# Kernel optimization log

Hardware: AMD Instinct MI355X
Metric: run time of the kernel (lower is better)

## Reference

```python
import jax, jax.numpy as jnp
import numpy as np

HEADS = 4
DIM_HEAD = 32
SCALE = DIM_HEAD ** -0.5


def setup_inputs() -> dict:
    key = jax.random.key(0)
    ks = jax.random.split(key, 7)
    b, c, h, w = 2, 256, 64, 64
    time_dim = 512
    hidden = HEADS * DIM_HEAD  # 128
    return {
        "x": jax.random.normal(ks[0], (b, c, h, w), jnp.float32),
        "time_emb": jax.random.normal(ks[1], (b, time_dim), jnp.float32),
        "w_mlp": jax.random.normal(ks[2], (2 * c, time_dim), jnp.float32) * 0.02,
        "b_mlp": jax.random.normal(ks[3], (2 * c,), jnp.float32) * 0.02,
        "w_qkv": jax.random.normal(ks[4], (3 * hidden, c), jnp.float32) * 0.05,
        "w_out": jax.random.normal(ks[5], (c, hidden), jnp.float32) * 0.05,
        "b_out": jax.random.normal(ks[6], (c,), jnp.float32) * 0.02,
    }


def reference(x, time_emb, w_mlp, b_mlp, w_qkv, w_out, b_out):
    b, c, h, w = x.shape
    n = h * w
    # FiLM conditioning: SiLU -> Linear -> chunk into (scale, shift)
    t = jax.nn.silu(time_emb) @ w_mlp.T + b_mlp            # [b, 2c]
    scale, shift = jnp.split(t, 2, axis=1)                  # [b, c] each
    x = x * (scale + 1.0)[:, :, None, None] + shift[:, :, None, None]
    # 1x1 conv QKV projection (no bias)
    qkv = jnp.einsum('oc,bchw->bohw', w_qkv, x)             # [b, 3*hidden, h, w]
    q, k, v = jnp.split(qkv, 3, axis=1)                     # [b, hidden, h, w]
    def to_heads(t):
        return t.reshape(b, HEADS, DIM_HEAD, n)             # b h d (x y)
    q, k, v = to_heads(q) * SCALE, to_heads(k), to_heads(v)
    sim = jnp.einsum('bhdi,bhdj->bhij', q, k)               # [b, h, n, n]
    attn = jax.nn.softmax(sim, axis=-1)
    out = jnp.einsum('bhij,bhdj->bhid', attn, v)            # [b, h, n, d]
    # b h (x y) d -> b (h d) x y
    out = out.transpose(0, 1, 3, 2).reshape(b, HEADS * DIM_HEAD, h, w)
    return jnp.einsum('oc,bchw->bohw', w_out, out) + b_out[None, :, None, None]
```

## Files before the change

kernel.cpp:

```cpp
#include <hip/hip_runtime.h>


typedef __bf16 bf16x8 __attribute__((ext_vector_type(8)));
typedef float  f32x16 __attribute__((ext_vector_type(16)));
typedef unsigned uint2v __attribute__((ext_vector_type(2)));

#define MFMA(a, b, c) __builtin_amdgcn_mfma_f32_32x32x16_bf16((a), (b), (c), 0, 0, 0)
#define PLSWAP(a, b) __builtin_amdgcn_permlane32_swap((a), (b), false, false)

static constexpr float kLOG2E = 1.4426950408889634f;
static constexpr float kSCALE = 0.17677669529663687f;

__device__ __forceinline__ unsigned short bf16r(float x) {
  union { float f; unsigned u; } v; v.f = x;
  return (unsigned short)((v.u + 0x7FFFu + ((v.u >> 16) & 1u)) >> 16);
}
__device__ __forceinline__ float fast_silu(float x) {
  return x / (1.0f + __builtin_amdgcn_exp2f(-x * kLOG2E));
}
__device__ __forceinline__ f32x16 zero16() {
  f32x16 z;
#pragma unroll
  for (int i = 0; i < 16; ++i) z[i] = 0.0f;
  return z;
}
__device__ __forceinline__ bf16x8 ld_frag(const unsigned short* p) {
  return *reinterpret_cast<const bf16x8*>(p);
}
__device__ __forceinline__ bf16x8 ld_lds_frag(const unsigned short* p) {
  union { unsigned long long q[2]; bf16x8 v; } u;
  u.q[0] = *(const unsigned long long*)(p);
  u.q[1] = *(const unsigned long long*)(p + 4);
  return u.v;
}

__global__ __launch_bounds__(256) void prep(const float* __restrict__ x,
                                            unsigned short* __restrict__ xT,
                                            const float* __restrict__ te,
                                            const float* __restrict__ w_mlp,
                                            const float* __restrict__ b_mlp,
                                            float* __restrict__ fparams) {
  __shared__ unsigned short lds[64][66];
  int bid = blockIdx.x;
  if (bid < 32) {
    int g = bid * 256 + threadIdx.x;
    int pair = g >> 3, ks = g & 7;
    int b = pair >> 9, o = pair & 511;
    const float4* w4 = (const float4*)(w_mlp + (size_t)o * 512 + ks * 64);
    const float4* t4 = (const float4*)(te + (size_t)b * 512 + ks * 64);
    float s = 0.0f;
#pragma unroll 4
    for (int k = 0; k < 16; ++k) {
      float4 wv = w4[k];
      float4 tv = t4[k];
      s += wv.x * fast_silu(tv.x) + wv.y * fast_silu(tv.y) +
           wv.z * fast_silu(tv.z) + wv.w * fast_silu(tv.w);
    }
    s += __shfl_xor(s, 1, 64);
    s += __shfl_xor(s, 2, 64);
    s += __shfl_xor(s, 4, 64);
    if (ks == 0) {
      float t_val = s + b_mlp[o];
      fparams[b * 512 + o] = (o < 256) ? (t_val + 1.0f) : t_val;
    }
    return;
  }
  int bid2 = bid - 32;
  int p0 = (bid2 & 63) * 64;
  int c0 = ((bid2 >> 6) & 3) * 64;
  int b  = bid2 >> 8;
  int t = threadIdx.x;
  int pl = t & 63, cw = t >> 6;
  const float* xb = x + ((size_t)b * 256 + c0) * 4096 + p0;
#pragma unroll
  for (int r = 0; r < 16; ++r) {
    int cl = cw + r * 4;
    lds[pl][cl] = bf16r(xb[(size_t)cl * 4096 + pl]);
  }
  __syncthreads();
  unsigned short* out = xT + ((size_t)b * 4096 + p0) * 256 + c0;
#pragma unroll
  for (int rep = 0; rep < 2; ++rep) {
    int ch = t + rep * 256;
    int pr = ch >> 3, cc = (ch & 7) * 8;
    union { unsigned short u[8]; uint4 v; } pk;
#pragma unroll
    for (int i = 0; i < 8; ++i) pk.u[i] = lds[pr][cc + i];
    *(uint4*)(out + (size_t)pr * 256 + cc) = pk.v;
  }
}

__global__ __launch_bounds__(256) void film2(const float* __restrict__ w_qkv,
                                             const float* __restrict__ fparams,
                                             const float* __restrict__ w_out,
                                             unsigned short* __restrict__ Aeff,
                                             float* __restrict__ qb,
                                             unsigned short* __restrict__ WoBf) {
  int tid = blockIdx.x * 256 + threadIdx.x;
  if (tid < 24576) {
    int row = tid >> 5, cs = tid & 31;
    int b = row / 384, o = row % 384;
    float qs = (o < 128) ? (kSCALE * kLOG2E) : 1.0f;
    const float4* wr  = (const float4*)(w_qkv + (size_t)o * 256);
    const float4* sc4 = (const float4*)(fparams + b * 512);
    const float4* sh4 = (const float4*)(fparams + b * 512 + 256);
    unsigned short* arow = Aeff + ((size_t)b * 384 + o) * 256;
    float acc = 0.0f;
#pragma unroll
    for (int j = 0; j < 2; ++j) {
      int c4 = cs * 2 + j;
      float4 wv = wr[c4], scv = sc4[c4], shv = sh4[c4];
      acc += wv.x * shv.x + wv.y * shv.y + wv.z * shv.z + wv.w * shv.w;
      union { unsigned short u[4]; unsigned long long q; } pk;
      pk.u[0] = bf16r(wv.x * scv.x * qs);
      pk.u[1] = bf16r(wv.y * scv.y * qs);
      pk.u[2] = bf16r(wv.z * scv.z * qs);
      pk.u[3] = bf16r(wv.w * scv.w * qs);
      *(unsigned long long*)(arow + c4 * 4) = pk.q;
    }
    acc += __shfl_xor(acc, 1, 64);
    acc += __shfl_xor(acc, 2, 64);
    acc += __shfl_xor(acc, 4, 64);
    acc += __shfl_xor(acc, 8, 64);
    acc += __shfl_xor(acc, 16, 64);
    if (cs == 0) qb[b * 384 + o] = acc * qs;
  } else {
    int t = tid - 24576;
    const float4* src = (const float4*)(w_out + (size_t)t * 64);
    unsigned short* dst = WoBf + (size_t)t * 64;
#pragma unroll 4
    for (int i = 0; i < 16; ++i) {
      float4 v = src[i];
      union { unsigned short u[4]; unsigned long long q; } pk;
      pk.u[0] = bf16r(v.x); pk.u[1] = bf16r(v.y);
      pk.u[2] = bf16r(v.z); pk.u[3] = bf16r(v.w);
      *(unsigned long long*)(dst + i * 4) = pk.q;
    }
  }
}

__global__ __launch_bounds__(64) void qkv_gemm(const unsigned short* __restrict__ Aeff,
                                               const float* __restrict__ qb,
                                               const unsigned short* __restrict__ xT,
                                               unsigned short* __restrict__ Qb,
                                               unsigned short* __restrict__ Kb,
                                               unsigned short* __restrict__ Vt) {
  int bid = blockIdx.x;
  int o_blk = bid % 12;
  int rest = bid / 12;
  int b = rest & 1, p_blk = rest >> 1;
  int l = threadIdx.x, col = l & 31, hi = l >> 5;

  const unsigned short* Ab = Aeff + ((size_t)b * 384 + o_blk * 32) * 256;
  const unsigned short* Bb = xT + ((size_t)b * 4096 + p_blk * 32) * 256;

  f32x16 acc = zero16();
#pragma unroll
  for (int kc = 0; kc < 256; kc += 16) {
    bf16x8 a0 = ld_frag(Ab + (size_t)col * 256 + kc + hi * 8);
    bf16x8 b0 = ld_frag(Bb + (size_t)col * 256 + kc + hi * 8);
    acc = MFMA(a0, b0, acc);
  }

  int obase = o_blk * 32;
  int sec = obase >> 7;
  int head = (obase & 127) >> 5;
  size_t bh = (size_t)b * 4 + head;
  int p = p_blk * 32 + col;
  if (sec < 2) {
    unsigned short* dst = (sec == 0 ? Qb : Kb) + (bh * 4096 + p) * 32;
#pragma unroll
    for (int g = 0; g < 4; ++g) {
      int dbase = 8 * g + 4 * hi;
      union { unsigned short u[4]; unsigned long long q; } pk;
#pragma unroll
      for (int r = 0; r < 4; ++r)
        pk.u[r] = bf16r(acc[4 * g + r] + qb[b * 384 + obase + dbase + r]);
      *(unsigned long long*)(dst + dbase) = pk.q;
    }
  } else {
    unsigned short* dst = Vt + bh * 131072 + (size_t)p_blk * 1024;
#pragma unroll
    for (int reg = 0; reg < 16; ++reg) {
      int d = (reg & 3) + 8 * (reg >> 2) + 4 * hi;
      dst[d * 32 + col] = bf16r(acc[reg] + qb[b * 384 + obase + d]);
    }
  }
}

__device__ __forceinline__ void softmax_pv(f32x16 S, bf16x8 va0, bf16x8 va1,
                                           f32x16& O, float& lsum) {
#pragma unroll
  for (int i = 0; i < 16; ++i) S[i] = __builtin_amdgcn_exp2f(S[i]);
  float s0 = (S[0] + S[1]) + (S[2] + S[3]);
  float s1 = (S[4] + S[5]) + (S[6] + S[7]);
  float s2 = (S[8] + S[9]) + (S[10] + S[11]);
  float s3 = (S[12] + S[13]) + (S[14] + S[15]);
  lsum += (s0 + s1) + (s2 + s3);
  union { __bf16 h[16]; unsigned u[8]; } pu;
#pragma unroll
  for (int i = 0; i < 16; ++i) pu.h[i] = (__bf16)S[i];
  uint2v r0 = PLSWAP(pu.u[0], pu.u[2]);
  uint2v r1 = PLSWAP(pu.u[1], pu.u[3]);
  uint2v r2 = PLSWAP(pu.u[4], pu.u[6]);
  uint2v r3 = PLSWAP(pu.u[5], pu.u[7]);
  union { unsigned u[4]; bf16x8 v; } B0, B1;
  B0.u[0] = r0[0]; B0.u[1] = r1[0]; B0.u[2] = r0[1]; B0.u[3] = r1[1];
  B1.u[0] = r2[0]; B1.u[1] = r3[0]; B1.u[2] = r2[1]; B1.u[3] = r3[1];
  O = MFMA(va0, B0.v, O);
  O = MFMA(va1, B1.v, O);
}

__global__ __launch_bounds__(256, 4) void attn(const unsigned short* __restrict__ Qb,
                                               const unsigned short* __restrict__ Kb,
                                               const unsigned short* __restrict__ Vt,
                                               float* __restrict__ Opart,
                                               float* __restrict__ Lpart) {
  __shared__ unsigned short kv[2][2][32][36];

  int bid = blockIdx.x;
  int qblk = bid & 15;
  int ks   = (bid >> 4) & 7;
  int bh   = bid >> 7;
  int t = threadIdx.x;
  int w = t >> 6, l = t & 63, col = l & 31, hi = l >> 5;

  int q0 = qblk * 256 + w * 64;
  const unsigned short* Qp = Qb + ((size_t)bh * 4096 + q0) * 32;
  bf16x8 qf0 = ld_frag(Qp + col * 32 + hi * 8);
  bf16x8 qf1 = ld_frag(Qp + col * 32 + 16 + hi * 8);
  bf16x8 qg0 = ld_frag(Qp + (col + 32) * 32 + hi * 8);
  bf16x8 qg1 = ld_frag(Qp + (col + 32) * 32 + 16 + hi * 8);

  int sec = t >> 7, rr = (t & 127) >> 2, cc = t & 3;
  const unsigned short* gsrc =
      (sec ? Vt : Kb) + (size_t)bh * 131072 + ks * 16384 + (t & 127) * 8;

  const f32x16 zc = zero16();
  f32x16 Oa = zero16(), Obb = zero16();
  float lsuma = 0.0f, lsumb = 0.0f;

  uint4 greg = *(const uint4*)(gsrc);

  for (int tt = 0; tt < 16; ++tt) {
    __syncthreads();
    int buf = tt & 1;
    unsigned short* d0 = &kv[buf][sec][rr][cc * 8];
    *(unsigned long long*)(d0)     = ((const unsigned long long*)&greg)[0];
    *(unsigned long long*)(d0 + 4) = ((const unsigned long long*)&greg)[1];
    if (tt < 15) greg = *(const uint4*)(gsrc + (tt + 1) * 1024);
    __syncthreads();

    bf16x8 ka0 = ld_lds_frag(&kv[buf][0][col][hi * 8]);
    bf16x8 ka1 = ld_lds_frag(&kv[buf][0][col][16 + hi * 8]);
    bf16x8 va0 = ld_lds_frag(&kv[buf][1][col][hi * 8]);
    bf16x8 va1 = ld_lds_frag(&kv[buf][1][col][16 + hi * 8]);

    f32x16 Sa = MFMA(ka0, qf0, zc);
    Sa = MFMA(ka1, qf1, Sa);
    softmax_pv(Sa, va0, va1, Oa, lsuma);

    f32x16 Sb = MFMA(ka0, qg0, zc);
    Sb = MFMA(ka1, qg1, Sb);
    softmax_pv(Sb, va0, va1, Obb, lsumb);
  }

  uint2v lra = PLSWAP(__float_as_uint(lsuma), __float_as_uint(lsuma));
  uint2v lrb = PLSWAP(__float_as_uint(lsumb), __float_as_uint(lsumb));
  float lta = __uint_as_float(lra[0]) + __uint_as_float(lra[1]);
  float ltb = __uint_as_float(lrb[0]) + __uint_as_float(lrb[1]);

  float* op = Opart + (size_t)(bh * 8 + ks) * 131072;
  float* lp = Lpart + (size_t)(bh * 8 + ks) * 4096;
#pragma unroll
  for (int r = 0; r < 16; ++r) {
    int d = (r & 3) + 8 * (r >> 2) + 4 * hi;
    op[d * 4096 + q0 + col]      = Oa[r];
    op[d * 4096 + q0 + 32 + col] = Obb[r];
  }
  if (hi == 0) {
    lp[q0 + col]      = lta;
    lp[q0 + 32 + col] = ltb;
  }
}

__global__ __launch_bounds__(256) void attn_merge(const float* __restrict__ Opart,
                                                  const float* __restrict__ Lpart,
                                                  unsigned short* __restrict__ Ob) {
  int idx = blockIdx.x * 256 + threadIdx.x;
  int dp = idx & 15;
  int q  = (idx >> 4) & 4095;
  int bh = idx >> 16;
  float s0 = 0.0f, s1 = 0.0f, L = 0.0f;
#pragma unroll
  for (int ks = 0; ks < 8; ++ks) {
    const float* op = Opart + (size_t)(bh * 8 + ks) * 131072;
    s0 += op[(2 * dp) * 4096 + q];
    s1 += op[(2 * dp + 1) * 4096 + q];
    L  += Lpart[(size_t)(bh * 8 + ks) * 4096 + q];
  }
  float inv = 1.0f / L;
  union { unsigned short u[2]; unsigned v; } pk;
  pk.u[0] = bf16r(s0 * inv);
  pk.u[1] = bf16r(s1 * inv);
  *(unsigned*)(Ob + ((size_t)bh * 4096 + q) * 32 + 2 * dp) = pk.v;
}

__global__ __launch_bounds__(64) void out_gemm(const unsigned short* __restrict__ Wo,
                                               const unsigned short* __restrict__ Ob,
                                               const float* __restrict__ b_out,
                                               float* __restrict__ out) {
  int bid = blockIdx.x;
  int o_blk = bid & 7;
  int rest = bid >> 3;
  int b = rest & 1, p_blk = rest >> 1;
  int l = threadIdx.x, col = l & 31, hi = l >> 5;

  const unsigned short* Ab = Wo + (size_t)(o_blk * 32) * 128;
  f32x16 acc = zero16();
#pragma unroll
  for (int kc = 0; kc < 128; kc += 16) {
    int head = kc >> 5;
    int doff = (kc & 16) + hi * 8;
    const unsigned short* Bb =
        Ob + (((size_t)b * 4 + head) * 4096 + p_blk * 32) * 32 + doff;
    bf16x8 a0 = ld_frag(Ab + (size_t)col * 128 + kc + hi * 8);
    bf16x8 b0 = ld_frag(Bb + (size_t)col * 32);
    acc = MFMA(a0, b0, acc);
  }
  int p = p_blk * 32 + col;
#pragma unroll
  for (int reg = 0; reg < 16; ++reg) {
    int o = o_blk * 32 + (reg & 3) + 8 * (reg >> 2) + 4 * hi;
    out[((size_t)b * 256 + o) * 4096 + p] = acc[reg] + b_out[o];
  }
}

extern "C" void kernel_launch(void* const* d_in, const int* in_sizes, int n_in,
                              void* d_out, int out_size, void* d_ws, size_t ws_size,
                              hipStream_t stream) {
  const float* x     = (const float*)d_in[0];
  const float* te    = (const float*)d_in[1];
  const float* w_mlp = (const float*)d_in[2];
  const float* b_mlp = (const float*)d_in[3];
  const float* w_qkv = (const float*)d_in[4];
  const float* w_out = (const float*)d_in[5];
  const float* b_out = (const float*)d_in[6];

  char* ws = (char*)d_ws;
  float*          fparams = (float*)(ws + 0);
  float*          qb      = (float*)(ws + 4096);
  unsigned short* Aeff    = (unsigned short*)(ws + 8192);
  unsigned short* WoBf    = (unsigned short*)(ws + 401408);
  unsigned short* xT      = (unsigned short*)(ws + 466944);
  unsigned short* Qb      = (unsigned short*)(ws + 4661248);
  unsigned short* Kb      = (unsigned short*)(ws + 6758400);
  unsigned short* Vt      = (unsigned short*)(ws + 8855552);
  unsigned short* Ob      = (unsigned short*)(ws + 10952704);
  float*          Opart   = (float*)(ws + 13049856);
  float*          Lpart   = (float*)(ws + 46604288);
  float* out = (float*)d_out;

  hipLaunchKernelGGL(prep, dim3(544), dim3(256), 0, stream, x, xT, te, w_mlp,
                     b_mlp, fparams);
  hipLaunchKernelGGL(film2, dim3(98), dim3(256), 0, stream, w_qkv, fparams, w_out,
                     Aeff, qb, WoBf);
  hipLaunchKernelGGL(qkv_gemm, dim3(3072), dim3(64), 0, stream, Aeff, qb, xT, Qb, Kb, Vt);
  hipLaunchKernelGGL(attn, dim3(1024), dim3(256), 0, stream, Qb, Kb, Vt, Opart, Lpart);
  hipLaunchKernelGGL(attn_merge, dim3(2048), dim3(256), 0, stream, Opart, Lpart, Ob);
  hipLaunchKernelGGL(out_gemm, dim3(2048), dim3(64), 0, stream, WoBf, Ob, b_out, out);
}
```

Before: 148.7 us.

## Stage QKV/out GEMM tiles in swizzled LDS, rework attn LDS layout and merge indexing

The QKV and output projection GEMMs now use 256-thread blocks that stage 64x64 tiles in LDS with an XOR swizzle, so each loaded A/B row is reused by two waves instead of every 32x32 wave reading global memory on its own. The attention kernel's K/V LDS layout becomes [chunk][row][8] so each fragment is one 16-byte LDS read and each store one uint4. The merge kernel reorders its index mapping so q is the fastest-varying dimension, which makes the Opart and Lpart reads coalesced, while the Ob writes become strided. Bigger blocks with more LDS may lower occupancy, and the grid counts shrink.

Measured after the change: 133.0 us. 1.12x faster.

```diff
diff --git a/kernel.cpp b/kernel.cpp
--- a/kernel.cpp
+++ b/kernel.cpp
@@ -26,12 +26,6 @@
 }
 __device__ __forceinline__ bf16x8 ld_frag(const unsigned short* p) {
   return *reinterpret_cast<const bf16x8*>(p);
-}
-__device__ __forceinline__ bf16x8 ld_lds_frag(const unsigned short* p) {
-  union { unsigned long long q[2]; bf16x8 v; } u;
-  u.q[0] = *(const unsigned long long*)(p);
-  u.q[1] = *(const unsigned long long*)(p + 4);
-  return u.v;
 }
 
 __global__ __launch_bounds__(256) void prep(const float* __restrict__ x,
@@ -139,34 +133,53 @@
   }
 }
 
-__global__ __launch_bounds__(64) void qkv_gemm(const unsigned short* __restrict__ Aeff,
-                                               const float* __restrict__ qb,
-                                               const unsigned short* __restrict__ xT,
-                                               unsigned short* __restrict__ Qb,
-                                               unsigned short* __restrict__ Kb,
-                                               unsigned short* __restrict__ Vt) {
+__global__ __launch_bounds__(256) void qkv_gemm(const unsigned short* __restrict__ Aeff,
+                                                const float* __restrict__ qb,
+                                                const unsigned short* __restrict__ xT,
+                                                unsigned short* __restrict__ Qb,
+                                                unsigned short* __restrict__ Kb,
+                                                unsigned short* __restrict__ Vt) {
+  __shared__ unsigned short As[64 * 256];
+  __shared__ unsigned short Bs[64 * 256];
   int bid = blockIdx.x;
-  int o_blk = bid % 12;
-  int rest = bid / 12;
+  int o_blk = bid % 6;
+  int rest = bid / 6;
   int b = rest & 1, p_blk = rest >> 1;
-  int l = threadIdx.x, col = l & 31, hi = l >> 5;
-
-  const unsigned short* Ab = Aeff + ((size_t)b * 384 + o_blk * 32) * 256;
-  const unsigned short* Bb = xT + ((size_t)b * 4096 + p_blk * 32) * 256;
+  int t = threadIdx.x;
+
+  const unsigned short* Ag = Aeff + ((size_t)b * 384 + o_blk * 64) * 256;
+  const unsigned short* Bg = xT + ((size_t)b * 4096 + p_blk * 64) * 256;
+
+#pragma unroll
+  for (int ps = 0; ps < 8; ++ps) {
+    int cid = ps * 256 + t;
+    int row = cid >> 5, ci = cid & 31;
+    uint4 va = *(const uint4*)(Ag + row * 256 + ci * 8);
+    uint4 vb = *(const uint4*)(Bg + row * 256 + ci * 8);
+    int sci = ci ^ (row & 7);
+    *(uint4*)(As + row * 256 + sci * 8) = va;
+    *(uint4*)(Bs + row * 256 + sci * 8) = vb;
+  }
+  __syncthreads();
+
+  int w = t >> 6, l = t & 63, col = l & 31, hi = l >> 5;
+  int wo = w >> 1, wp = w & 1;
+  int ao = wo * 32 + col, bp = wp * 32 + col;
 
   f32x16 acc = zero16();
 #pragma unroll
   for (int kc = 0; kc < 256; kc += 16) {
-    bf16x8 a0 = ld_frag(Ab + (size_t)col * 256 + kc + hi * 8);
-    bf16x8 b0 = ld_frag(Bb + (size_t)col * 256 + kc + hi * 8);
+    int ch = (kc >> 3) + hi;
+    bf16x8 a0 = ld_frag(As + ao * 256 + (ch ^ (ao & 7)) * 8);
+    bf16x8 b0 = ld_frag(Bs + bp * 256 + (ch ^ (bp & 7)) * 8);
     acc = MFMA(a0, b0, acc);
   }
 
-  int obase = o_blk * 32;
+  int obase = o_blk * 64 + wo * 32;
   int sec = obase >> 7;
   int head = (obase & 127) >> 5;
   size_t bh = (size_t)b * 4 + head;
-  int p = p_blk * 32 + col;
+  int p = p_blk * 64 + wp * 32 + col;
   if (sec < 2) {
     unsigned short* dst = (sec == 0 ? Qb : Kb) + (bh * 4096 + p) * 32;
 #pragma unroll
@@ -179,11 +192,11 @@
       *(unsigned long long*)(dst + dbase) = pk.q;
     }
   } else {
-    unsigned short* dst = Vt + bh * 131072 + (size_t)p_blk * 1024;
+    unsigned short* dst = Vt + bh * 131072 + (size_t)(p >> 5) * 1024;
 #pragma unroll
     for (int reg = 0; reg < 16; ++reg) {
       int d = (reg & 3) + 8 * (reg >> 2) + 4 * hi;
-      dst[d * 32 + col] = bf16r(acc[reg] + qb[b * 384 + obase + d]);
+      dst[d * 32 + (p & 31)] = bf16r(acc[reg] + qb[b * 384 + obase + d]);
     }
   }
 }
@@ -216,7 +229,7 @@
                                                const unsigned short* __restrict__ Vt,
                                                float* __restrict__ Opart,
                                                float* __restrict__ Lpart) {
-  __shared__ unsigned short kv[2][2][32][36];
+  __shared__ unsigned short kv[2][2][4][32][8];
 
   int bid = blockIdx.x;
   int qblk = bid & 15;
@@ -232,9 +245,9 @@
   bf16x8 qg0 = ld_frag(Qp + (col + 32) * 32 + hi * 8);
   bf16x8 qg1 = ld_frag(Qp + (col + 32) * 32 + 16 + hi * 8);
 
-  int sec = t >> 7, rr = (t & 127) >> 2, cc = t & 3;
+  int sec = t >> 7, g = t & 127, rr = g >> 2, cc = g & 3;
   const unsigned short* gsrc =
-      (sec ? Vt : Kb) + (size_t)bh * 131072 + ks * 16384 + (t & 127) * 8;
+      (sec ? Vt : Kb) + (size_t)bh * 131072 + ks * 16384 + g * 8;
 
   const f32x16 zc = zero16();
   f32x16 Oa = zero16(), Obb = zero16();
@@ -245,16 +258,14 @@
   for (int tt = 0; tt < 16; ++tt) {
     __syncthreads();
     int buf = tt & 1;
-    unsigned short* d0 = &kv[buf][sec][rr][cc * 8];
-    *(unsigned long long*)(d0)     = ((const unsigned long long*)&greg)[0];
-    *(unsigned long long*)(d0 + 4) = ((const unsigned long long*)&greg)[1];
+    *(uint4*)(&kv[buf][sec][cc][rr][0]) = greg;
     if (tt < 15) greg = *(const uint4*)(gsrc + (tt + 1) * 1024);
     __syncthreads();
 
-    bf16x8 ka0 = ld_lds_frag(&kv[buf][0][col][hi * 8]);
-    bf16x8 ka1 = ld_lds_frag(&kv[buf][0][col][16 + hi * 8]);
-    bf16x8 va0 = ld_lds_frag(&kv[buf][1][col][hi * 8]);
-    bf16x8 va1 = ld_lds_frag(&kv[buf][1][col][16 + hi * 8]);
+    bf16x8 ka0 = ld_frag(&kv[buf][0][hi][col][0]);
+    bf16x8 ka1 = ld_frag(&kv[buf][0][2 + hi][col][0]);
+    bf16x8 va0 = ld_frag(&kv[buf][1][hi][col][0]);
+    bf16x8 va1 = ld_frag(&kv[buf][1][2 + hi][col][0]);
 
     f32x16 Sa = MFMA(ka0, qf0, zc);
     Sa = MFMA(ka1, qf1, Sa);
@@ -288,9 +299,10 @@
                                                   const float* __restrict__ Lpart,
                                                   unsigned short* __restrict__ Ob) {
   int idx = blockIdx.x * 256 + threadIdx.x;
-  int dp = idx & 15;
-  int q  = (idx >> 4) & 4095;
-  int bh = idx >> 16;
+  int q  = idx & 4095;
+  int rest = idx >> 12;
+  int dp = rest & 15;
+  int bh = rest >> 4;
   float s0 = 0.0f, s1 = 0.0f, L = 0.0f;
 #pragma unroll
   for (int ks = 0; ks < 8; ++ks) {
@@ -306,32 +318,50 @@
   *(unsigned*)(Ob + ((size_t)bh * 4096 + q) * 32 + 2 * dp) = pk.v;
 }
 
-__global__ __launch_bounds__(64) void out_gemm(const unsigned short* __restrict__ Wo,
-                                               const unsigned short* __restrict__ Ob,
-                                               const float* __restrict__ b_out,
-                                               float* __restrict__ out) {
+__global__ __launch_bounds__(256) void out_gemm(const unsigned short* __restrict__ Wo,
+                                                const unsigned short* __restrict__ Ob,
+                                                const float* __restrict__ b_out,
+                                                float* __restrict__ out) {
+  __shared__ unsigned short As[64 * 128];
+  __shared__ unsigned short Bs[64 * 128];
   int bid = blockIdx.x;
-  int o_blk = bid & 7;
-  int rest = bid >> 3;
+  int o_blk = bid & 3;
+  int rest = bid >> 2;
   int b = rest & 1, p_blk = rest >> 1;
-  int l = threadIdx.x, col = l & 31, hi = l >> 5;
-
-  const unsigned short* Ab = Wo + (size_t)(o_blk * 32) * 128;
+  int t = threadIdx.x;
+  int p0 = p_blk * 64;
+
+  const unsigned short* Ag = Wo + (size_t)(o_blk * 64) * 128;
+#pragma unroll
+  for (int ps = 0; ps < 4; ++ps) {
+    int cid = ps * 256 + t;
+    int row = cid >> 4, ci = cid & 15;
+    uint4 va = *(const uint4*)(Ag + row * 128 + ci * 8);
+    int head = ci >> 2, dch = ci & 3;
+    uint4 vb = *(const uint4*)(Ob + (((size_t)b * 4 + head) * 4096 + p0 + row) * 32 +
+                               dch * 8);
+    int sci = ci ^ (row & 7);
+    *(uint4*)(As + row * 128 + sci * 8) = va;
+    *(uint4*)(Bs + row * 128 + sci * 8) = vb;
+  }
+  __syncthreads();
+
+  int w = t >> 6, l = t & 63, col = l & 31, hi = l >> 5;
+  int wo = w >> 1, wp = w & 1;
+  int ao = wo * 32 + col, bp = wp * 32 + col;
+
   f32x16 acc = zero16();
 #pragma unroll
   for (int kc = 0; kc < 128; kc += 16) {
-    int head = kc >> 5;
-    int doff = (kc & 16) + hi * 8;
-    const unsigned short* Bb =
-        Ob + (((size_t)b * 4 + head) * 4096 + p_blk * 32) * 32 + doff;
-    bf16x8 a0 = ld_frag(Ab + (size_t)col * 128 + kc + hi * 8);
-    bf16x8 b0 = ld_frag(Bb + (size_t)col * 32);
+    int ch = (kc >> 3) + hi;
+    bf16x8 a0 = ld_frag(As + ao * 128 + ((ch ^ (ao & 7)) & 15) * 8);
+    bf16x8 b0 = ld_frag(Bs + bp * 128 + ((ch ^ (bp & 7)) & 15) * 8);
     acc = MFMA(a0, b0, acc);
   }
-  int p = p_blk * 32 + col;
+  int p = p0 + wp * 32 + col;
 #pragma unroll
   for (int reg = 0; reg < 16; ++reg) {
-    int o = o_blk * 32 + (reg & 3) + 8 * (reg >> 2) + 4 * hi;
+    int o = o_blk * 64 + wo * 32 + (reg & 3) + 8 * (reg >> 2) + 4 * hi;
     out[((size_t)b * 256 + o) * 4096 + p] = acc[reg] + b_out[o];
   }
 }
@@ -365,8 +395,8 @@
                      b_mlp, fparams);
   hipLaunchKernelGGL(film2, dim3(98), dim3(256), 0, stream, w_qkv, fparams, w_out,
                      Aeff, qb, WoBf);
-  hipLaunchKernelGGL(qkv_gemm, dim3(3072), dim3(64), 0, stream, Aeff, qb, xT, Qb, Kb, Vt);
+  hipLaunchKernelGGL(qkv_gemm, dim3(768), dim3(256), 0, stream, Aeff, qb, xT, Qb, Kb, Vt);
   hipLaunchKernelGGL(attn, dim3(1024), dim3(256), 0, stream, Qb, Kb, Vt, Opart, Lpart);
   hipLaunchKernelGGL(attn_merge, dim3(2048), dim3(256), 0, stream, Opart, Lpart, Ob);
-  hipLaunchKernelGGL(out_gemm, dim3(2048), dim3(64), 0, stream, WoBf, Ob, b_out, out);
-}
+  hipLaunchKernelGGL(out_gemm, dim3(512), dim3(256), 0, stream, WoBf, Ob, b_out, out);
+}
```
